# Performance work log

Measured on AMD Instinct MI355X. Metric: run time of the kernel, lower is better.

The kernel has to match this reference:

```python
import jax, jax.numpy as jnp
import numpy as np

HEAD = 8

def setup_inputs() -> dict:
    key = jax.random.key(0)
    ks = jax.random.split(key, 11)
    B, C, W, H = 16, 512, 32, 32
    d, N = C // HEAD, W * H
    return {
        "x": jax.random.normal(ks[0], (B, C, W, H), jnp.float32),
        "Wq": jax.random.normal(ks[1], (C, C), jnp.float32) * 0.02,
        "bq": jax.random.normal(ks[2], (C,), jnp.float32) * 0.02,
        "Wk": jax.random.normal(ks[3], (C, C), jnp.float32) * 0.02,
        "bk": jax.random.normal(ks[4], (C,), jnp.float32) * 0.02,
        "Wv": jax.random.normal(ks[5], (C, C), jnp.float32) * 0.02,
        "bv": jax.random.normal(ks[6], (C,), jnp.float32) * 0.02,
        "rel_h": jax.random.normal(ks[7], (1, HEAD, d, 1, H), jnp.float32),
        "rel_w": jax.random.normal(ks[8], (1, HEAD, d, W, 1), jnp.float32),
        "reg_qk": jax.random.normal(ks[9], (1, N, N), jnp.float32),
        "reg_v": jax.random.normal(ks[10], (1, d, N), jnp.float32),
    }

def reference(x, Wq, bq, Wk, bk, Wv, bv, rel_h, rel_w, reg_qk, reg_v):
    B, C, W, H = x.shape
    head = HEAD
    d = C // head
    N = W * H
    def conv1x1(inp, Wt, b):  # 1x1 conv == per-pixel linear
        return jnp.einsum('bchw,oc->bohw', inp, Wt) + b[None, :, None, None]
    q = conv1x1(x, Wq, bq).reshape(B, head, d, N)
    k = conv1x1(x, Wk, bk).reshape(B, head, d, N)
    v = conv1x1(x, Wv, bv).reshape(B, head, d, N)
    # content-content: q^T k -> [B, head, N, N]
    cc = jnp.einsum('bhdn,bhdm->bhnm', q, k)
    # content-position: (rel_h + rel_w) broadcast to [1, head, d, W, H] -> [head, N, d]
    pos = (rel_h + rel_w).reshape(head, d, N)
    cp = jnp.einsum('hdn,bhdm->bhnm', pos, q)
    energy = cc + cp  # [B, head, N, N]
    n_reg = reg_qk.shape[0]
    energy = jnp.concatenate(
        [energy, jnp.broadcast_to(reg_qk[None], (B, n_reg, N, N))], axis=1)
    v_all = jnp.concatenate(
        [v, jnp.broadcast_to(reg_v[None], (B, n_reg, d, N))], axis=1)
    attn = jax.nn.softmax(energy, axis=-1)  # [B, head+n_reg, N, N]
    # v @ attn^T
    out = jnp.einsum('bgdn,bgmn->bgdm', v_all, attn)
    out = out[:, :head].reshape(B, C, W, H)
    return out + x
```

## Files before the change

### kernel.cpp

```cpp
#include <hip/hip_runtime.h>

#define BB   16
#define HEADS 8
#define DH   64
#define NSP  1024
#define CCH  512

typedef unsigned int   u32;
typedef unsigned short u16;
typedef __attribute__((ext_vector_type(8))) short  short8;
typedef __attribute__((ext_vector_type(4))) float  floatx4;
typedef __attribute__((ext_vector_type(2))) unsigned uint2v;

#if defined(__has_builtin)
#if __has_builtin(__builtin_amdgcn_exp2f)
#define EXP2F(x) __builtin_amdgcn_exp2f(x)
#else
#define EXP2F(x) exp2f(x)
#endif
#if __has_builtin(__builtin_amdgcn_permlane32_swap)
#define HAVE_PL32 1
#endif
#if __has_builtin(__builtin_amdgcn_permlane16_swap)
#define HAVE_PL16 1
#endif
#else
#define EXP2F(x) exp2f(x)
#endif

__device__ __forceinline__ u16 f2b(float f) {
  u32 x = __float_as_uint(f);
  x = x + 0x7fffu + ((x >> 16) & 1u);
  return (u16)(x >> 16);
}

__device__ __forceinline__ u32 pkbf(float lo, float hi) {
  return __builtin_amdgcn_perm(__float_as_uint(hi) + 0x8000u,
                               __float_as_uint(lo) + 0x8000u, 0x07060302u);
}

__device__ __forceinline__ void gload_lds16(const u16* g, u16* l) {
  __builtin_amdgcn_global_load_lds((const __attribute__((address_space(1))) u32*)g,
                                   (__attribute__((address_space(3))) u32*)l, 16, 0, 0);
}

__device__ __forceinline__ void lane32_swap(u32 a, u32 b, u32& ap, u32& bp, bool hi32) {
#ifdef HAVE_PL32
  uint2v r = __builtin_amdgcn_permlane32_swap(a, b, false, false);
  ap = r.x; bp = r.y;
  (void)hi32;
#else
  u32 sb = (u32)__shfl_xor((int)b, 32);
  u32 sa = (u32)__shfl_xor((int)a, 32);
  ap = hi32 ? sb : a;
  bp = hi32 ? b : sa;
#endif
}

__device__ __forceinline__ u32 lane16_xor(u32 x, bool qodd) {
#ifdef HAVE_PL16
  uint2v r = __builtin_amdgcn_permlane16_swap(x, x, false, false);
  return qodd ? r.x : r.y;
#else
  return (u32)__shfl_xor((int)x, 16);
#endif
}


__global__ __launch_bounds__(256) void prep_all(const float* __restrict__ x,
                                                const float* __restrict__ Wq,
                                                const float* __restrict__ Wk,
                                                const float* __restrict__ Wv,
                                                const float* __restrict__ rel_h,
                                                const float* __restrict__ rel_w,
                                                u16* __restrict__ wbf,
                                                u16* __restrict__ pos,
                                                u16* __restrict__ xt) {
  __shared__ float ld[64][68];
  int bid = blockIdx.x;
  int t = threadIdx.x;
  if (bid < 768) {
    int idx = bid * 256 + t;
    int which = idx >> 16;
    int r4 = (idx & 65535) * 4;
    const float* src = which == 0 ? Wq : which == 1 ? Wk : Wv;
    float4 v = *(const float4*)&src[r4];
    ushort4 s;
    s.x = f2b(v.x); s.y = f2b(v.y); s.z = f2b(v.z); s.w = f2b(v.w);
    *(ushort4*)&wbf[(which << 18) + r4] = s;
  } else if (bid < 2816) {
    int idx = (bid - 768) * 256 + t;
    int dd = idx & 63;
    int n  = (idx >> 6) & 1023;
    int hd = idx >> 16;
    int ww = n >> 5, hh = n & 31;
    float v = rel_h[(hd * 64 + dd) * 32 + hh] + rel_w[(hd * 64 + dd) * 32 + ww];
    int ntp = n >> 6, nbp = (n >> 4) & 3, rp = n & 15;
    int ksp = dd >> 5, qp = (dd >> 3) & 3, ep = dd & 7;
    size_t off = ((((size_t)(hd * 16 + ntp) * 4 + nbp) * 2 + ksp) * 64 + qp * 16 + rp) * 8 + ep;
    pos[off] = f2b(v);
  } else {
    int bid2 = bid - 2816;
    int ntile = bid2 & 15, ctile = (bid2 >> 4) & 7, b = bid2 >> 7;
    const float* xb = x + (((size_t)b * CCH + ctile * 64) << 10) + ntile * 64;
#pragma unroll
    for (int p = 0; p < 4; ++p) {
      int c = p * 16 + (t >> 4), n4 = (t & 15) * 4;
      float4 v = *(const float4*)&xb[((size_t)c << 10) + n4];
      ld[c][n4 + 0] = v.x; ld[c][n4 + 1] = v.y; ld[c][n4 + 2] = v.z; ld[c][n4 + 3] = v.w;
    }
    __syncthreads();
    u16* xo = xt + (((size_t)b << 10) + ntile * 64) * CCH + ctile * 64;
#pragma unroll
    for (int p = 0; p < 2; ++p) {
      int id = p * 256 + t;
      int n = id >> 3, c8 = (id & 7) * 8;
      ushort4 s0, s1;
      s0.x = f2b(ld[c8 + 0][n]); s0.y = f2b(ld[c8 + 1][n]);
      s0.z = f2b(ld[c8 + 2][n]); s0.w = f2b(ld[c8 + 3][n]);
      s1.x = f2b(ld[c8 + 4][n]); s1.y = f2b(ld[c8 + 5][n]);
      s1.z = f2b(ld[c8 + 6][n]); s1.w = f2b(ld[c8 + 7][n]);
      *(ushort4*)&xo[(size_t)n * CCH + c8] = s0;
      *(ushort4*)&xo[(size_t)n * CCH + c8 + 4] = s1;
    }
  }
}

__global__ __launch_bounds__(256, 2) void qkv_fused(const u16* __restrict__ wbf,
                                                    const u16* __restrict__ xt,
                                                    const float* __restrict__ bq,
                                                    const float* __restrict__ bk,
                                                    const float* __restrict__ bv,
                                                    u16* __restrict__ qw,
                                                    u16* __restrict__ kw,
                                                    u16* __restrict__ vtw) {
  int hid = blockIdx.x;
  int xcd  = hid & 7;
  int slot = hid >> 3;
  int otile = slot & 7;
  int pair  = xcd * 16 + (slot >> 3);
  int ntile = pair & 7;
  int b     = pair >> 3;
  int o0 = otile * 64, n0 = ntile * 128;

  __shared__ __align__(16) u16 smem[2 * 20480];

  int t = threadIdx.x;
  int w = t >> 6, lane = t & 63;
  int l15 = lane & 15, quad = lane >> 4;
  int srow = lane >> 3, sc = lane & 7;
  int scc = (sc ^ srow) << 3;

  floatx4 aq[8], ak[8], av[8];
#pragma unroll
  for (int i = 0; i < 8; ++i) {
    aq[i] = (floatx4){0.f, 0.f, 0.f, 0.f};
    ak[i] = (floatx4){0.f, 0.f, 0.f, 0.f};
    av[i] = (floatx4){0.f, 0.f, 0.f, 0.f};
  }

  auto stage = [&](int k0, int buf) {
    u16* base = smem + buf * 20480;
#pragma unroll
    for (int p = 0; p < 10; ++p) {
      int g0 = w * 80 + p * 8;
      if (g0 < 192) {
        int which = g0 >> 6;
        int r0 = g0 & 63;
        gload_lds16(wbf + ((size_t)which << 18) + (size_t)(o0 + r0 + srow) * CCH + k0 + scc,
                    base + which * 4096 + r0 * 64);
      } else {
        int r0 = g0 - 192;
        gload_lds16(xt + (size_t)(b * 1024 + n0 + r0 + srow) * CCH + k0 + scc,
                    base + 12288 + r0 * 64);
      }
    }
  };

  int rs = l15 & 7;
  int c0 = (quad ^ rs) << 3;
  int c1 = ((4 + quad) ^ rs) << 3;
  int wrow = (w * 16 + l15) * 64;

  stage(0, 0);
  stage(64, 1);

  for (int ki = 0; ki < 8; ++ki) {
    if (ki < 7) asm volatile("s_waitcnt vmcnt(10)" ::: "memory");
    else        asm volatile("s_waitcnt vmcnt(0)" ::: "memory");
    __builtin_amdgcn_s_barrier();
    __builtin_amdgcn_sched_barrier(0);

    u16* base = smem + (ki & 1) * 20480;
    u16* Xb = base + 12288;
#pragma unroll
    for (int ks = 0; ks < 2; ++ks) {
      int cc = ks ? c1 : c0;
      short8 fq = *(short8*)&base[wrow + cc];
      short8 fk = *(short8*)&base[4096 + wrow + cc];
      short8 fv = *(short8*)&base[8192 + wrow + cc];
#pragma unroll
      for (int ns = 0; ns < 8; ++ns) {
        short8 fx = *(short8*)&Xb[(ns * 16 + l15) * 64 + cc];
        aq[ns] = __builtin_amdgcn_mfma_f32_16x16x32_bf16(fq, fx, aq[ns], 0, 0, 0);
        ak[ns] = __builtin_amdgcn_mfma_f32_16x16x32_bf16(fk, fx, ak[ns], 0, 0, 0);
        av[ns] = __builtin_amdgcn_mfma_f32_16x16x32_bf16(fx, fv, av[ns], 0, 0, 0);
      }
    }

    if (ki < 6) {
      __builtin_amdgcn_sched_barrier(0);
      __builtin_amdgcn_s_barrier();
      stage((ki + 2) * 64, ki & 1);
    }
  }

  __syncthreads();
  u16* epQ = smem;
  u16* epK = smem + 9216;
  u16* epV = smem + 18432;
  {
    int ob = o0 + w * 16 + quad * 4;
    float q0 = bq[ob], q1 = bq[ob + 1], q2 = bq[ob + 2], q3 = bq[ob + 3];
    float k0b = bk[ob], k1b = bk[ob + 1], k2b = bk[ob + 2], k3b = bk[ob + 3];
    float vb = bv[o0 + w * 16 + l15];
#pragma unroll
    for (int ns = 0; ns < 8; ++ns) {
      int n = ns * 16 + l15;
      uint2 pk;
      pk.x = pkbf(aq[ns][0] + q0, aq[ns][1] + q1);
      pk.y = pkbf(aq[ns][2] + q2, aq[ns][3] + q3);
      *(uint2*)&epQ[n * 72 + w * 16 + quad * 4] = pk;
      pk.x = pkbf(ak[ns][0] + k0b, ak[ns][1] + k1b);
      pk.y = pkbf(ak[ns][2] + k2b, ak[ns][3] + k3b);
      *(uint2*)&epK[n * 72 + w * 16 + quad * 4] = pk;
      pk.x = pkbf(av[ns][0] + vb, av[ns][1] + vb);
      pk.y = pkbf(av[ns][2] + vb, av[ns][3] + vb);
      *(uint2*)&epV[(w * 16 + l15) * 136 + ns * 16 + quad * 4] = pk;
    }
  }
  __syncthreads();
  int h = otile;
  size_t bhI = (size_t)(b * HEADS + h);
  {
    int row = t >> 1, half = t & 1;
    int nt_ = (n0 + row) >> 6;
    int nblk_ = (row >> 4) & 3;
    int r_ = row & 15;
    size_t qkbase = (((bhI * 16 + nt_) * 4 + nblk_) * 2 + half) * 512;
#pragma unroll
    for (int i = 0; i < 4; ++i)
      *(uint4*)&qw[qkbase + (i * 16 + r_) * 8] = *(uint4*)&epQ[row * 72 + half * 32 + i * 8];
#pragma unroll
    for (int i = 0; i < 4; ++i)
      *(uint4*)&kw[qkbase + (i * 16 + r_) * 8] = *(uint4*)&epK[row * 72 + half * 32 + i * 8];
  }
  {
    int row = t >> 2, q4 = t & 3;
    int ddblk = row >> 4, r_ = row & 15;
#pragma unroll
    for (int i = 0; i < 4; ++i) {
      int nl = q4 * 32 + i * 8;
      int n = n0 + nl;
      int ntv = n >> 6, np = n & 63;
      int nh = np >> 5, q = (np >> 3) & 3;
      size_t vbase = (((bhI * 16 + ntv) * 4 + ddblk) * 2 + nh) * 512;
      *(uint4*)&vtw[vbase + (q * 16 + r_) * 8] = *(uint4*)&epV[row * 136 + nl];
    }
  }
}

__global__ __launch_bounds__(256, 2) void attn_mfma(const u16* __restrict__ qw,
                                                    const u16* __restrict__ kw,
                                                    const u16* __restrict__ vtw,
                                                    const u16* __restrict__ pos,
                                                    const float* __restrict__ x,
                                                    float* __restrict__ out) {
  int bh = blockIdx.x, mtile = blockIdx.y;
  int b = bh >> 3, h = bh & 7;
  __shared__ __align__(16) float smem_f[9216];

  int t = threadIdx.x;
  int w = t >> 6, lane = t & 63;
  int l15 = lane & 15, quad = lane >> 4;
  bool qodd = (quad & 1) != 0;
  bool hi32 = lane >= 32;
  size_t bhs = (size_t)bh;
  int lane8 = lane * 8;

  short8 qa[4][2], pa[4][2];
  {
    const u16* qmb = qw + bhs * 65536 + (size_t)(mtile * 4 + w) * 4096;
    const u16* pmb = pos + (size_t)h * 65536 + (size_t)(mtile * 4 + w) * 4096;
#pragma unroll
    for (int msub = 0; msub < 4; ++msub)
#pragma unroll
      for (int ks = 0; ks < 2; ++ks) {
        int off = (msub * 2 + ks) * 512 + lane8;
        qa[msub][ks] = *(const short8*)(qmb + off);
        pa[msub][ks] = *(const short8*)(pmb + off);
      }
  }

  floatx4 oacc[4][4];
  float lsum[4] = {0.f, 0.f, 0.f, 0.f};
#pragma unroll
  for (int i = 0; i < 4; ++i)
#pragma unroll
    for (int j = 0; j < 4; ++j) oacc[i][j] = (floatx4){0.f, 0.f, 0.f, 0.f};

  const u16* kg = kw + bhs * 65536;
  const u16* qg = qw + bhs * 65536;
  const u16* vg = vtw + bhs * 65536;

  for (int nt = 0; nt < 16; ++nt) {
    const u16* kgt = kg + nt * 4096;
    const u16* qgt = qg + nt * 4096;
    const u16* vgt = vg + nt * 4096;

    short8 kb[4][2], qb[4][2], vb[4][2];
#pragma unroll
    for (int nblk = 0; nblk < 4; ++nblk)
#pragma unroll
      for (int ks = 0; ks < 2; ++ks) {
        int off = (nblk * 2 + ks) * 512 + lane8;
        kb[nblk][ks] = *(const short8*)(kgt + off);
        qb[nblk][ks] = *(const short8*)(qgt + off);
      }
#pragma unroll
    for (int dd = 0; dd < 4; ++dd)
#pragma unroll
      for (int hf = 0; hf < 2; ++hf)
        vb[dd][hf] = *(const short8*)(vgt + (dd * 2 + hf) * 512 + lane8);

#pragma unroll
    for (int half = 0; half < 2; ++half) {
      u32 Wd[4][4];
#pragma unroll
      for (int nblk2 = 0; nblk2 < 2; ++nblk2) {
        int nblk = half * 2 + nblk2;
        floatx4 sc4[4];
#pragma unroll
        for (int msub = 0; msub < 4; ++msub) {
          floatx4 c = (floatx4){0.f, 0.f, 0.f, 0.f};
          c = __builtin_amdgcn_mfma_f32_16x16x32_bf16(kb[nblk][0], qa[msub][0], c, 0, 0, 0);
          c = __builtin_amdgcn_mfma_f32_16x16x32_bf16(kb[nblk][1], qa[msub][1], c, 0, 0, 0);
          c = __builtin_amdgcn_mfma_f32_16x16x32_bf16(qb[nblk][0], pa[msub][0], c, 0, 0, 0);
          c = __builtin_amdgcn_mfma_f32_16x16x32_bf16(qb[nblk][1], pa[msub][1], c, 0, 0, 0);
          sc4[msub] = c;
        }
#pragma unroll
        for (int msub = 0; msub < 4; ++msub) {
          float p0 = EXP2F(fmaf(sc4[msub][0], 1.44269504f, -11.5415603f));
          float p1 = EXP2F(fmaf(sc4[msub][1], 1.44269504f, -11.5415603f));
          float p2 = EXP2F(fmaf(sc4[msub][2], 1.44269504f, -11.5415603f));
          float p3 = EXP2F(fmaf(sc4[msub][3], 1.44269504f, -11.5415603f));
          lsum[msub] += (p0 + p1) + (p2 + p3);
          Wd[msub][nblk2 * 2 + 0] = pkbf(p0, p1);
          Wd[msub][nblk2 * 2 + 1] = pkbf(p2, p3);
        }
      }
      short8 pB[4];
#pragma unroll
      for (int msub = 0; msub < 4; ++msub) {
        u32 A0p, B0p, A1p, B1p;
        lane32_swap(Wd[msub][0], Wd[msub][2], A0p, B0p, hi32);
        lane32_swap(Wd[msub][1], Wd[msub][3], A1p, B1p, hi32);
        u32 G0 = lane16_xor(qodd ? A0p : B0p, qodd);
        u32 G1 = lane16_xor(qodd ? A1p : B1p, qodd);
        union { u32 u[4]; short8 s; } cvt;
        cvt.u[0] = qodd ? G0 : A0p;
        cvt.u[1] = qodd ? G1 : A1p;
        cvt.u[2] = qodd ? B0p : G0;
        cvt.u[3] = qodd ? B1p : G1;
        pB[msub] = cvt.s;
      }
#pragma unroll
      for (int dd = 0; dd < 4; ++dd) {
#pragma unroll
        for (int msub = 0; msub < 4; ++msub)
          oacc[msub][dd] = __builtin_amdgcn_mfma_f32_16x16x32_bf16(vb[dd][half], pB[msub], oacc[msub][dd], 0, 0, 0);
      }
    }
  }

  float rinv[4];
#pragma unroll
  for (int msub = 0; msub < 4; ++msub) {
    float l = lsum[msub];
    l += __shfl_xor(l, 16);
    l += __shfl_xor(l, 32);
    rinv[msub] = 1.0f / l;
  }

  float* ot = smem_f + w * 2304;
  int l8 = lane & 7, lr = lane >> 3;
#pragma unroll
  for (int mh = 0; mh < 2; ++mh) {
#pragma unroll
    for (int ms2 = 0; ms2 < 2; ++ms2) {
      int msub = mh * 2 + ms2;
#pragma unroll
      for (int dd = 0; dd < 4; ++dd)
#pragma unroll
        for (int r = 0; r < 4; ++r)
          ot[(dd * 16 + quad * 4 + r) * 36 + ms2 * 16 + l15] = oacc[msub][dd][r] * rinv[msub];
    }
#pragma unroll
    for (int pass = 0; pass < 8; ++pass) {
      int dd = pass * 8 + lr;
      float4 o4 = *(float4*)&ot[dd * 36 + l8 * 4];
      size_t off = (((size_t)b * CCH + h * DH + dd) << 10) + mtile * 256 + w * 64 + mh * 32 + l8 * 4;
      float4 xv = *(const float4*)&x[off];
      o4.x += xv.x; o4.y += xv.y; o4.z += xv.z; o4.w += xv.w;
      *(float4*)&out[off] = o4;
    }
  }
}

extern "C" void kernel_launch(void* const* d_in, const int* in_sizes, int n_in,
                              void* d_out, int out_size, void* d_ws, size_t ws_size,
                              hipStream_t stream) {
  const float* x     = (const float*)d_in[0];
  const float* Wq    = (const float*)d_in[1];
  const float* bq    = (const float*)d_in[2];
  const float* Wk    = (const float*)d_in[3];
  const float* bk    = (const float*)d_in[4];
  const float* Wv    = (const float*)d_in[5];
  const float* bv    = (const float*)d_in[6];
  const float* rel_h = (const float*)d_in[7];
  const float* rel_w = (const float*)d_in[8];
  float* out = (float*)d_out;

  char* ws = (char*)d_ws;
  u16* qw   = (u16*)(ws);
  u16* kw   = (u16*)(ws + ((size_t)16 << 20));
  u16* vtw  = (u16*)(ws + ((size_t)32 << 20));
  u16* pos  = (u16*)(ws + ((size_t)48 << 20));
  u16* wbf  = (u16*)(ws + ((size_t)49 << 20));
  u16* xt   = (u16*)d_out;

  hipLaunchKernelGGL(prep_all, dim3(4864), dim3(256), 0, stream,
                     x, Wq, Wk, Wv, rel_h, rel_w, wbf, pos, xt);
  hipLaunchKernelGGL(qkv_fused, dim3(1024), dim3(256), 0, stream,
                     wbf, xt, bq, bk, bv, qw, kw, vtw);
  hipLaunchKernelGGL(attn_mfma, dim3(128, 4), dim3(256), 0, stream,
                     qw, kw, vtw, pos, x, out);
}
```

Measured before the change: 199.3 us.

## Double-buffer K/Q fragment loads across half-tiles with software prefetch

Splits each key tile into two halves with separate register buffers for the K and Q fragments. The next half's loads are issued before computing the current half, with scheduling barriers placed between them, so global load latency overlaps the MFMA and exp work. V loads move inside each half. On the last iteration the prefetch redundantly reloads tile 15, and the extra live buffers add register pressure while the barriers limit the compiler's freedom to reorder.

```diff
diff --git a/kernel.cpp b/kernel.cpp
--- a/kernel.cpp
+++ b/kernel.cpp
@@ -313,76 +313,95 @@
   const u16* qg = qw + bhs * 65536;
   const u16* vg = vtw + bhs * 65536;
 
+  short8 kA[2][2], qA[2][2], kB[2][2], qB[2][2];
+
+#define LOADKQ(KBUF, QBUF, kt_, qt_, hf)                                  \
+  {                                                                        \
+    _Pragma("unroll")                                                      \
+    for (int nb2 = 0; nb2 < 2; ++nb2) {                                    \
+      _Pragma("unroll")                                                    \
+      for (int ks = 0; ks < 2; ++ks) {                                     \
+        int off = (((hf) * 2 + nb2) * 2 + ks) * 512 + lane8;               \
+        KBUF[nb2][ks] = *(const short8*)((kt_) + off);                     \
+        QBUF[nb2][ks] = *(const short8*)((qt_) + off);                     \
+      }                                                                    \
+    }                                                                      \
+  }
+
+#define COMPUTEH(KBUF, QBUF, vt_, hf)                                      \
+  {                                                                        \
+    short8 vb[4];                                                          \
+    _Pragma("unroll")                                                      \
+    for (int dd = 0; dd < 4; ++dd)                                         \
+      vb[dd] = *(const short8*)((vt_) + (dd * 2 + (hf)) * 512 + lane8);    \
+    u32 Wd[4][4];                                                          \
+    _Pragma("unroll")                                                      \
+    for (int nblk2 = 0; nblk2 < 2; ++nblk2) {                              \
+      floatx4 sc4[4];                                                      \
+      _Pragma("unroll")                                                    \
+      for (int msub = 0; msub < 4; ++msub) {                               \
+        floatx4 c = (floatx4){0.f, 0.f, 0.f, 0.f};                         \
+        c = __builtin_amdgcn_mfma_f32_16x16x32_bf16(KBUF[nblk2][0], qa[msub][0], c, 0, 0, 0); \
+        c = __builtin_amdgcn_mfma_f32_16x16x32_bf16(KBUF[nblk2][1], qa[msub][1], c, 0, 0, 0); \
+        c = __builtin_amdgcn_mfma_f32_16x16x32_bf16(QBUF[nblk2][0], pa[msub][0], c, 0, 0, 0); \
+        c = __builtin_amdgcn_mfma_f32_16x16x32_bf16(QBUF[nblk2][1], pa[msub][1], c, 0, 0, 0); \
+        sc4[msub] = c;                                                     \
+      }                                                                    \
+      _Pragma("unroll")                                                    \
+      for (int msub = 0; msub < 4; ++msub) {                               \
+        float p0 = EXP2F(fmaf(sc4[msub][0], 1.44269504f, -11.5415603f));   \
+        float p1 = EXP2F(fmaf(sc4[msub][1], 1.44269504f, -11.5415603f));   \
+        float p2 = EXP2F(fmaf(sc4[msub][2], 1.44269504f, -11.5415603f));   \
+        float p3 = EXP2F(fmaf(sc4[msub][3], 1.44269504f, -11.5415603f));   \
+        lsum[msub] += (p0 + p1) + (p2 + p3);                               \
+        Wd[msub][nblk2 * 2 + 0] = pkbf(p0, p1);                            \
+        Wd[msub][nblk2 * 2 + 1] = pkbf(p2, p3);                            \
+      }                                                                    \
+    }                                                                      \
+    short8 pB[4];                                                          \
+    _Pragma("unroll")                                                      \
+    for (int msub = 0; msub < 4; ++msub) {                                 \
+      u32 A0p, B0p, A1p, B1p;                                              \
+      lane32_swap(Wd[msub][0], Wd[msub][2], A0p, B0p, hi32);               \
+      lane32_swap(Wd[msub][1], Wd[msub][3], A1p, B1p, hi32);               \
+      u32 G0 = lane16_xor(qodd ? A0p : B0p, qodd);                         \
+      u32 G1 = lane16_xor(qodd ? A1p : B1p, qodd);                         \
+      union { u32 u[4]; short8 s; } cvt;                                   \
+      cvt.u[0] = qodd ? G0 : A0p;                                          \
+      cvt.u[1] = qodd ? G1 : A1p;                                          \
+      cvt.u[2] = qodd ? B0p : G0;                                          \
+      cvt.u[3] = qodd ? B1p : G1;                                          \
+      pB[msub] = cvt.s;                                                    \
+    }                                                                      \
+    _Pragma("unroll")                                                      \
+    for (int dd = 0; dd < 4; ++dd) {                                       \
+      _Pragma("unroll")                                                    \
+      for (int msub = 0; msub < 4; ++msub)                                 \
+        oacc[msub][dd] = __builtin_amdgcn_mfma_f32_16x16x32_bf16(vb[dd], pB[msub], oacc[msub][dd], 0, 0, 0); \
+    }                                                                      \
+  }
+
+  LOADKQ(kA, qA, kg, qg, 0);
+
   for (int nt = 0; nt < 16; ++nt) {
     const u16* kgt = kg + nt * 4096;
     const u16* qgt = qg + nt * 4096;
     const u16* vgt = vg + nt * 4096;
-
-    short8 kb[4][2], qb[4][2], vb[4][2];
-#pragma unroll
-    for (int nblk = 0; nblk < 4; ++nblk)
-#pragma unroll
-      for (int ks = 0; ks < 2; ++ks) {
-        int off = (nblk * 2 + ks) * 512 + lane8;
-        kb[nblk][ks] = *(const short8*)(kgt + off);
-        qb[nblk][ks] = *(const short8*)(qgt + off);
-      }
-#pragma unroll
-    for (int dd = 0; dd < 4; ++dd)
-#pragma unroll
-      for (int hf = 0; hf < 2; ++hf)
-        vb[dd][hf] = *(const short8*)(vgt + (dd * 2 + hf) * 512 + lane8);
-
-#pragma unroll
-    for (int half = 0; half < 2; ++half) {
-      u32 Wd[4][4];
-#pragma unroll
-      for (int nblk2 = 0; nblk2 < 2; ++nblk2) {
-        int nblk = half * 2 + nblk2;
-        floatx4 sc4[4];
-#pragma unroll
-        for (int msub = 0; msub < 4; ++msub) {
-          floatx4 c = (floatx4){0.f, 0.f, 0.f, 0.f};
-          c = __builtin_amdgcn_mfma_f32_16x16x32_bf16(kb[nblk][0], qa[msub][0], c, 0, 0, 0);
-          c = __builtin_amdgcn_mfma_f32_16x16x32_bf16(kb[nblk][1], qa[msub][1], c, 0, 0, 0);
-          c = __builtin_amdgcn_mfma_f32_16x16x32_bf16(qb[nblk][0], pa[msub][0], c, 0, 0, 0);
-          c = __builtin_amdgcn_mfma_f32_16x16x32_bf16(qb[nblk][1], pa[msub][1], c, 0, 0, 0);
-          sc4[msub] = c;
-        }
-#pragma unroll
-        for (int msub = 0; msub < 4; ++msub) {
-          float p0 = EXP2F(fmaf(sc4[msub][0], 1.44269504f, -11.5415603f));
-          float p1 = EXP2F(fmaf(sc4[msub][1], 1.44269504f, -11.5415603f));
-          float p2 = EXP2F(fmaf(sc4[msub][2], 1.44269504f, -11.5415603f));
-          float p3 = EXP2F(fmaf(sc4[msub][3], 1.44269504f, -11.5415603f));
-          lsum[msub] += (p0 + p1) + (p2 + p3);
-          Wd[msub][nblk2 * 2 + 0] = pkbf(p0, p1);
-          Wd[msub][nblk2 * 2 + 1] = pkbf(p2, p3);
-        }
-      }
-      short8 pB[4];
-#pragma unroll
-      for (int msub = 0; msub < 4; ++msub) {
-        u32 A0p, B0p, A1p, B1p;
-        lane32_swap(Wd[msub][0], Wd[msub][2], A0p, B0p, hi32);
-        lane32_swap(Wd[msub][1], Wd[msub][3], A1p, B1p, hi32);
-        u32 G0 = lane16_xor(qodd ? A0p : B0p, qodd);
-        u32 G1 = lane16_xor(qodd ? A1p : B1p, qodd);
-        union { u32 u[4]; short8 s; } cvt;
-        cvt.u[0] = qodd ? G0 : A0p;
-        cvt.u[1] = qodd ? G1 : A1p;
-        cvt.u[2] = qodd ? B0p : G0;
-        cvt.u[3] = qodd ? B1p : G1;
-        pB[msub] = cvt.s;
-      }
-#pragma unroll
-      for (int dd = 0; dd < 4; ++dd) {
-#pragma unroll
-        for (int msub = 0; msub < 4; ++msub)
-          oacc[msub][dd] = __builtin_amdgcn_mfma_f32_16x16x32_bf16(vb[dd][half], pB[msub], oacc[msub][dd], 0, 0, 0);
-      }
-    }
-  }
+    int ntn = nt < 15 ? nt + 1 : 15;
+    const u16* kgn = kg + ntn * 4096;
+    const u16* qgn = qg + ntn * 4096;
+
+    LOADKQ(kB, qB, kgt, qgt, 1);
+    __builtin_amdgcn_sched_barrier(0);
+    COMPUTEH(kA, qA, vgt, 0);
+
+    LOADKQ(kA, qA, kgn, qgn, 0);
+    __builtin_amdgcn_sched_barrier(0);
+    COMPUTEH(kB, qB, vgt, 1);
+  }
+
+#undef LOADKQ
+#undef COMPUTEH
 
   float rinv[4];
 #pragma unroll
```

After: 239.2 us. 20.0% more time.

## Stage K/Q/V tiles through triple-buffered LDS with async global-to-LDS loads

Applied to the files above, without the earlier changes.

Each block now cooperatively copies the K, Q and V tiles into a three-slot LDS ring using direct global-to-LDS loads, issued two tiles ahead and gated by explicit vmcnt waits and barriers. Previously every wave loaded its own full copy of each tile from global memory into registers. The change spreads the load work across the four waves and overlaps memory traffic with MFMA work. In exchange it adds per-iteration barriers and LDS reads, and grows LDS use to 72KB, which may limit how many blocks fit on a CU.

```diff
diff --git a/kernel.cpp b/kernel.cpp
--- a/kernel.cpp
+++ b/kernel.cpp
@@ -278,7 +278,7 @@
                                                     float* __restrict__ out) {
   int bh = blockIdx.x, mtile = blockIdx.y;
   int b = bh >> 3, h = bh & 7;
-  __shared__ __align__(16) float smem_f[9216];
+  __shared__ __align__(16) u16 smem_u16[36864];
 
   int t = threadIdx.x;
   int w = t >> 6, lane = t & 63;
@@ -313,25 +313,40 @@
   const u16* qg = qw + bhs * 65536;
   const u16* vg = vtw + bhs * 65536;
 
-  for (int nt = 0; nt < 16; ++nt) {
+  auto stage = [&](int nt, int buf) {
+    u16* kt = smem_u16 + buf * 12288;
+    u16* qt = kt + 4096;
+    u16* vt = qt + 4096;
     const u16* kgt = kg + nt * 4096;
     const u16* qgt = qg + nt * 4096;
     const u16* vgt = vg + nt * 4096;
-
-    short8 kb[4][2], qb[4][2], vb[4][2];
-#pragma unroll
-    for (int nblk = 0; nblk < 4; ++nblk)
-#pragma unroll
-      for (int ks = 0; ks < 2; ++ks) {
-        int off = (nblk * 2 + ks) * 512 + lane8;
-        kb[nblk][ks] = *(const short8*)(kgt + off);
-        qb[nblk][ks] = *(const short8*)(qgt + off);
-      }
-#pragma unroll
-    for (int dd = 0; dd < 4; ++dd)
-#pragma unroll
-      for (int hf = 0; hf < 2; ++hf)
-        vb[dd][hf] = *(const short8*)(vgt + (dd * 2 + hf) * 512 + lane8);
+#pragma unroll
+    for (int p = 0; p < 2; ++p) {
+      int o = w * 1024 + p * 512;
+      gload_lds16(kgt + o + lane8, kt + o);
+      gload_lds16(qgt + o + lane8, qt + o);
+      gload_lds16(vgt + o + lane8, vt + o);
+    }
+  };
+
+  stage(0, 0);
+  stage(1, 1);
+
+  for (int nt = 0; nt < 16; ++nt) {
+    __builtin_amdgcn_s_barrier();
+    if (nt < 14) {
+      stage(nt + 2, (nt + 2) % 3);
+      asm volatile("s_waitcnt vmcnt(12)" ::: "memory");
+    } else if (nt == 14) {
+      asm volatile("s_waitcnt vmcnt(6)" ::: "memory");
+    } else {
+      asm volatile("s_waitcnt vmcnt(0)" ::: "memory");
+    }
+    __builtin_amdgcn_sched_barrier(0);
+
+    u16* kt = smem_u16 + (nt % 3) * 12288;
+    u16* qt = kt + 4096;
+    u16* vt = qt + 4096;
 
 #pragma unroll
     for (int half = 0; half < 2; ++half) {
@@ -339,14 +354,18 @@
 #pragma unroll
       for (int nblk2 = 0; nblk2 < 2; ++nblk2) {
         int nblk = half * 2 + nblk2;
+        short8 kb0 = *(short8*)&kt[(nblk * 2 + 0) * 512 + lane8];
+        short8 kb1 = *(short8*)&kt[(nblk * 2 + 1) * 512 + lane8];
+        short8 qb0 = *(short8*)&qt[(nblk * 2 + 0) * 512 + lane8];
+        short8 qb1 = *(short8*)&qt[(nblk * 2 + 1) * 512 + lane8];
         floatx4 sc4[4];
 #pragma unroll
         for (int msub = 0; msub < 4; ++msub) {
           floatx4 c = (floatx4){0.f, 0.f, 0.f, 0.f};
-          c = __builtin_amdgcn_mfma_f32_16x16x32_bf16(kb[nblk][0], qa[msub][0], c, 0, 0, 0);
-          c = __builtin_amdgcn_mfma_f32_16x16x32_bf16(kb[nblk][1], qa[msub][1], c, 0, 0, 0);
-          c = __builtin_amdgcn_mfma_f32_16x16x32_bf16(qb[nblk][0], pa[msub][0], c, 0, 0, 0);
-          c = __builtin_amdgcn_mfma_f32_16x16x32_bf16(qb[nblk][1], pa[msub][1], c, 0, 0, 0);
+          c = __builtin_amdgcn_mfma_f32_16x16x32_bf16(kb0, qa[msub][0], c, 0, 0, 0);
+          c = __builtin_amdgcn_mfma_f32_16x16x32_bf16(kb1, qa[msub][1], c, 0, 0, 0);
+          c = __builtin_amdgcn_mfma_f32_16x16x32_bf16(qb0, pa[msub][0], c, 0, 0, 0);
+          c = __builtin_amdgcn_mfma_f32_16x16x32_bf16(qb1, pa[msub][1], c, 0, 0, 0);
           sc4[msub] = c;
         }
 #pragma unroll
@@ -377,9 +396,10 @@
       }
 #pragma unroll
       for (int dd = 0; dd < 4; ++dd) {
+        short8 vb = *(short8*)&vt[(dd * 2 + half) * 512 + lane8];
 #pragma unroll
         for (int msub = 0; msub < 4; ++msub)
-          oacc[msub][dd] = __builtin_amdgcn_mfma_f32_16x16x32_bf16(vb[dd][half], pB[msub], oacc[msub][dd], 0, 0, 0);
+          oacc[msub][dd] = __builtin_amdgcn_mfma_f32_16x16x32_bf16(vb, pB[msub], oacc[msub][dd], 0, 0, 0);
       }
     }
   }
@@ -393,7 +413,8 @@
     rinv[msub] = 1.0f / l;
   }
 
-  float* ot = smem_f + w * 2304;
+  __syncthreads();
+  float* ot = (float*)smem_u16 + w * 2304;
   int l8 = lane & 7, lr = lane >> 3;
 #pragma unroll
   for (int mh = 0; mh < 2; ++mh) {
```

Result: no change. 197.3 us (-1.0%).
